# Kernel optimization log

Hardware: AMD Instinct MI355X
Metric: run time of the kernel (lower is better)

The kernel has to match this reference:

```python
import jax, jax.numpy as jnp
import numpy as np

B, N, EDGES = 16, 50000, 1600000
CLAMP_MIN, CLAMP_MAX = -10.0, 10.0
EPS = 1e-6


def setup_inputs() -> dict:
    key = jax.random.key(0)
    ks = jax.random.split(key, 8)
    return {
        "chem_influence": jax.random.normal(ks[0], (B, N), dtype=jnp.float32),
        "E": jax.random.normal(ks[1], (B, N), dtype=jnp.float32),
        "o_pre": jax.random.uniform(ks[2], (B, N), dtype=jnp.float32),
        "w": jax.random.normal(ks[3], (EDGES,), dtype=jnp.float32),
        "threshold": jax.random.uniform(ks[4], (N,), dtype=jnp.float32),
        "decay": jax.random.uniform(ks[5], (N,), dtype=jnp.float32),
        "src": jax.random.randint(ks[6], (EDGES,), 0, N, dtype=jnp.int32),
        "dst": jax.random.randint(ks[7], (EDGES,), 0, N, dtype=jnp.int32),
    }


def reference(chem_influence, E, o_pre, w, threshold, decay, src, dst):
    # Gap-junction currents: gather, sign-compare, weighted scatter-add.
    Oj = o_pre[:, src]                      # (B, EDGES) presynaptic outputs
    En = E[:, dst]                          # (B, EDGES) postsynaptic internal states
    sgn = jnp.where(Oj >= En, 1.0, -1.0)
    contrib = Oj * w * sgn                  # (B, EDGES)
    gj_sum = jnp.zeros_like(chem_influence).at[:, dst].add(contrib)  # (B, N)

    # Neuron dynamics (eqs 10, 11).
    S = jnp.clip(E + chem_influence + gj_sum, CLAMP_MIN, CLAMP_MAX)
    gt = S > threshold                      # broadcast (N,) over (B, N)
    mask = (~gt) & (jnp.abs(S - E) <= EPS)
    new_o = jax.nn.relu(S - threshold)
    new_e = jnp.where(gt, new_o, jnp.where(mask, E - decay, S))
    return (new_o, new_e)
```

## Files before the change

### kernel.cpp

```cpp
#include <hip/hip_runtime.h>

#define BATCH 16
#define NNODES 50000
#define NEDGES 1600000
#define BN (BATCH * NNODES)
#define CLAMP_LO -10.0f
#define CLAMP_HI 10.0f
#define EPS_V 1e-6f

#define BSZ 64
#define NBINS 782
#define CAPE 2816
#define RPT 11
#define NBLK_P 391
#define EPB 4096

__global__ __launch_bounds__(256) void prep_fused(
    const float* __restrict__ o_pre, const float* __restrict__ E,
    const int* __restrict__ src, const int* __restrict__ dst,
    const float* __restrict__ w,
    float* __restrict__ o_t, float* __restrict__ E_t,
    uint2* __restrict__ binned, int* __restrict__ gcur) {
    __shared__ int lh[NBINS];
    const int tid = threadIdx.x, bid = blockIdx.x;
    for (int i = tid; i < NBINS; i += 256) lh[i] = 0;

    const int4*   dst4 = (const int4*)dst;
    const int4*   src4 = (const int4*)src;
    const float4* w4   = (const float4*)w;
    const int e4base = bid * (EPB / 4);
    int4 d[4], s[4];
    float4 ww[4];
    bool val[4];
#pragma unroll
    for (int j = 0; j < 4; ++j) {
        int i4 = e4base + j * 256 + tid;
        val[j] = (i4 * 4 < NEDGES);
        if (val[j]) { d[j] = dst4[i4]; s[j] = src4[i4]; ww[j] = w4[i4]; }
    }

    if (tid < 128) {
        int t = bid * 128 + tid;
        if (t < NNODES) {
            float v[BATCH], u[BATCH];
#pragma unroll
            for (int b = 0; b < BATCH; ++b) {
                v[b] = o_pre[b * NNODES + t];
                u[b] = E[b * NNODES + t];
            }
            float4* op = (float4*)(o_t + (size_t)t * BATCH);
            float4* ep = (float4*)(E_t + (size_t)t * BATCH);
#pragma unroll
            for (int k = 0; k < 4; ++k) {
                op[k] = make_float4(v[4*k], v[4*k+1], v[4*k+2], v[4*k+3]);
                ep[k] = make_float4(u[4*k], u[4*k+1], u[4*k+2], u[4*k+3]);
            }
        }
    }
    __syncthreads();

#pragma unroll
    for (int j = 0; j < 4; ++j) {
        if (val[j]) {
            atomicAdd(&lh[d[j].x >> 6], 1);
            atomicAdd(&lh[d[j].y >> 6], 1);
            atomicAdd(&lh[d[j].z >> 6], 1);
            atomicAdd(&lh[d[j].w >> 6], 1);
        }
    }
    __syncthreads();

    for (int i = tid; i < NBINS; i += 256) {
        int c = lh[i];
        int base = c ? atomicAdd(&gcur[i], c) : 0;
        lh[i] = i * CAPE + base;
    }
    __syncthreads();

#pragma unroll
    for (int j = 0; j < 4; ++j) {
        if (val[j]) {
            int   dd[4] = {d[j].x, d[j].y, d[j].z, d[j].w};
            int   ss[4] = {s[j].x, s[j].y, s[j].z, s[j].w};
            float wv[4] = {ww[j].x, ww[j].y, ww[j].z, ww[j].w};
#pragma unroll
            for (int m = 0; m < 4; ++m) {
                int dn  = dd[m];
                int bin = dn >> 6;
                int pos = atomicAdd(&lh[bin], 1);
                if (pos < (bin + 1) * CAPE)
                    binned[pos] = make_uint2(
                        (unsigned)ss[m] | ((unsigned)(dn & 63) << 16),
                        __float_as_uint(wv[m]));
            }
        }
    }
}

__global__ __launch_bounds__(256, 4) void bin_gather6(
    const float* __restrict__ o_t, const float* __restrict__ E_t,
    const float* __restrict__ chem, const float* __restrict__ threshold,
    const float* __restrict__ decay, const int* __restrict__ gcur,
    const uint2* __restrict__ binned,
    float* __restrict__ out_o, float* __restrict__ out_e) {
    __shared__ int   cnt_l[BSZ];
    __shared__ int   offs[BSZ + 1];
    __shared__ uint2 eb[CAPE];
    const int k = blockIdx.x, tid = threadIdx.x;
    const int node0 = k * BSZ;
    const int nn = (NNODES - node0 < BSZ) ? (NNODES - node0) : BSZ;
    const int s0 = k * CAPE;
    int cnt = gcur[k];
    if (cnt > CAPE) cnt = CAPE;

    uint2 r[RPT];
    if (tid < BSZ) cnt_l[tid] = 0;
    __syncthreads();
#pragma unroll
    for (int j = 0; j < RPT; ++j) {
        int idx = tid + j * 256;
        if (idx < cnt) {
            uint2 p = binned[s0 + idx];
            r[j] = p;
            atomicAdd(&cnt_l[(p.x >> 16) & 63], 1);
        }
    }
    __syncthreads();

    if (tid < BSZ) {
        int c = cnt_l[tid];
        int v = c;
#pragma unroll
        for (int o = 1; o < BSZ; o <<= 1) {
            int u = __shfl_up(v, o);
            if (tid >= o) v += u;
        }
        offs[tid]  = v - c;
        cnt_l[tid] = v - c;
        if (tid == BSZ - 1) offs[BSZ] = cnt;
    }
    __syncthreads();

#pragma unroll
    for (int j = 0; j < RPT; ++j) {
        int idx = tid + j * 256;
        if (idx < cnt) {
            uint2 p = r[j];
            int pos = atomicAdd(&cnt_l[(p.x >> 16) & 63], 1);
            eb[pos] = p;
        }
    }
    __syncthreads();

    if (tid < nn * 4) {
        const int n  = tid >> 2;
        const int q  = (tid & 3) * 4;
        const int gn = node0 + n;
        const int e0 = offs[n], e1 = offs[n + 1];
        const float4 en = *(const float4*)(E_t + (size_t)gn * BATCH + q);
        const float th = threshold[gn];
        const float dc = decay[gn];
        float ch[4];
#pragma unroll
        for (int j = 0; j < 4; ++j) ch[j] = chem[(q + j) * NNODES + gn];

        float4 acc = make_float4(0.f, 0.f, 0.f, 0.f);
        int i = e0;
        for (; i + 2 <= e1; i += 2) {
            uint2 p0 = eb[i];
            uint2 p1 = eb[i + 1];
            float4 oj0 = *(const float4*)(o_t + (size_t)(p0.x & 0xFFFFu) * BATCH + q);
            float4 oj1 = *(const float4*)(o_t + (size_t)(p1.x & 0xFFFFu) * BATCH + q);
            float w0 = __uint_as_float(p0.y), nw0 = -w0;
            float w1 = __uint_as_float(p1.y), nw1 = -w1;
            acc.x = fmaf(oj0.x, (oj0.x >= en.x) ? w0 : nw0, acc.x);
            acc.y = fmaf(oj0.y, (oj0.y >= en.y) ? w0 : nw0, acc.y);
            acc.z = fmaf(oj0.z, (oj0.z >= en.z) ? w0 : nw0, acc.z);
            acc.w = fmaf(oj0.w, (oj0.w >= en.w) ? w0 : nw0, acc.w);
            acc.x = fmaf(oj1.x, (oj1.x >= en.x) ? w1 : nw1, acc.x);
            acc.y = fmaf(oj1.y, (oj1.y >= en.y) ? w1 : nw1, acc.y);
            acc.z = fmaf(oj1.z, (oj1.z >= en.z) ? w1 : nw1, acc.z);
            acc.w = fmaf(oj1.w, (oj1.w >= en.w) ? w1 : nw1, acc.w);
        }
        if (i < e1) {
            uint2 p0 = eb[i];
            float4 oj0 = *(const float4*)(o_t + (size_t)(p0.x & 0xFFFFu) * BATCH + q);
            float w0 = __uint_as_float(p0.y), nw0 = -w0;
            acc.x = fmaf(oj0.x, (oj0.x >= en.x) ? w0 : nw0, acc.x);
            acc.y = fmaf(oj0.y, (oj0.y >= en.y) ? w0 : nw0, acc.y);
            acc.z = fmaf(oj0.z, (oj0.z >= en.z) ? w0 : nw0, acc.z);
            acc.w = fmaf(oj0.w, (oj0.w >= en.w) ? w0 : nw0, acc.w);
        }

        float ev[4] = {en.x, en.y, en.z, en.w};
        float av[4] = {acc.x, acc.y, acc.z, acc.w};
#pragma unroll
        for (int j = 0; j < 4; ++j) {
            float e = ev[j];
            float S = e + ch[j] + av[j];
            S = fminf(fmaxf(S, CLAMP_LO), CLAMP_HI);
            float no = fmaxf(S - th, 0.0f);
            float ne;
            if (S > th) ne = no;
            else if (fabsf(S - e) <= EPS_V) ne = e - dc;
            else ne = S;
            out_o[(q + j) * NNODES + gn] = no;
            out_e[(q + j) * NNODES + gn] = ne;
        }
    }
}

__global__ void edge_scatter_dev(const float* __restrict__ o_pre, const float* __restrict__ E,
                                 const float* __restrict__ w, const int* __restrict__ src,
                                 const int* __restrict__ dst, float* __restrict__ gj) {
    int e = blockIdx.x * blockDim.x + threadIdx.x;
    if (e >= NEDGES) return;
    int s = src[e];
    int d = dst[e];
    float wv = w[e];
#pragma unroll
    for (int b = 0; b < BATCH; ++b) {
        float oj = o_pre[b * NNODES + s];
        float en = E[b * NNODES + d];
        atomicAdd(&gj[b * NNODES + d], (oj >= en) ? oj * wv : -oj * wv);
    }
}

__global__ void finalize_dev(const float* __restrict__ chem, const float* __restrict__ E,
                             const float* __restrict__ threshold, const float* __restrict__ decay,
                             float* __restrict__ out_o, float* __restrict__ out_e_gj) {
    int i = blockIdx.x * blockDim.x + threadIdx.x;
    if (i >= BN) return;
    int n = i % NNODES;
    float e = E[i];
    float S = e + chem[i] + out_e_gj[i];
    S = fminf(fmaxf(S, CLAMP_LO), CLAMP_HI);
    float th = threshold[n];
    float no = fmaxf(S - th, 0.0f);
    float ne;
    if (S > th) ne = no;
    else if (fabsf(S - e) <= EPS_V) ne = e - decay[n];
    else ne = S;
    out_o[i] = no;
    out_e_gj[i] = ne;
}

extern "C" void kernel_launch(void* const* d_in, const int* in_sizes, int n_in,
                              void* d_out, int out_size, void* d_ws, size_t ws_size,
                              hipStream_t stream) {
    const float* chem      = (const float*)d_in[0];
    const float* E         = (const float*)d_in[1];
    const float* o_pre     = (const float*)d_in[2];
    const float* w         = (const float*)d_in[3];
    const float* threshold = (const float*)d_in[4];
    const float* decay     = (const float*)d_in[5];
    const int*   src       = (const int*)d_in[6];
    const int*   dst       = (const int*)d_in[7];

    float* out_o = (float*)d_out;
    float* out_e = (float*)d_out + BN;

    const size_t OT_OFF  = 0;
    const size_t ET_OFF  = 3203072;
    const size_t BIN_OFF = 6406144;
    const size_t GC_OFF  = 24023040;
    const size_t need    = GC_OFF + (size_t)NBINS * sizeof(int);

    if (ws_size >= need) {
        char* ws = (char*)d_ws;
        float* o_t    = (float*)(ws + OT_OFF);
        float* E_t    = (float*)(ws + ET_OFF);
        uint2* binned = (uint2*)(ws + BIN_OFF);
        int*   gcur   = (int*)(ws + GC_OFF);

        hipMemsetAsync(gcur, 0, (size_t)NBINS * sizeof(int), stream);
        prep_fused<<<NBLK_P, 256, 0, stream>>>(o_pre, E, src, dst, w, o_t, E_t, binned, gcur);
        bin_gather6<<<NBINS, 256, 0, stream>>>(o_t, E_t, chem, threshold, decay,
                                               gcur, binned, out_o, out_e);
    } else {
        hipMemsetAsync(out_e, 0, (size_t)BN * sizeof(float), stream);
        edge_scatter_dev<<<(NEDGES + 255) / 256, 256, 0, stream>>>(o_pre, E, w, src, dst, out_e);
        finalize_dev<<<(BN + 255) / 256, 256, 0, stream>>>(chem, E, threshold, decay, out_o, out_e);
    }
}
```

Baseline: 125.3 us.

## Drop E transpose, read E directly in gather; halve edges per prep block

Removes the transposed copy of E from the prep kernel, so the gather kernel reads E from its original batch-major layout, the same way it already reads chem. The prep kernel now runs twice as many blocks with half the edges each, and all 256 threads take part in transposing o_pre, each writing a float4. The gather inner loop is unrolled by four edges to expose more independent loads. This saves one 3.2 MB write and its re-read, but the E reads in the gather become strided across batch rows, and the extra prep blocks mean more shared-histogram setup and more global bin atomics.

```diff
diff --git a/kernel.cpp b/kernel.cpp
--- a/kernel.cpp
+++ b/kernel.cpp
@@ -12,14 +12,14 @@
 #define NBINS 782
 #define CAPE 2816
 #define RPT 11
-#define NBLK_P 391
-#define EPB 4096
+#define NBLK_P 782
+#define EPB 2048
 
 __global__ __launch_bounds__(256) void prep_fused(
-    const float* __restrict__ o_pre, const float* __restrict__ E,
+    const float* __restrict__ o_pre,
     const int* __restrict__ src, const int* __restrict__ dst,
     const float* __restrict__ w,
-    float* __restrict__ o_t, float* __restrict__ E_t,
+    float* __restrict__ o_t,
     uint2* __restrict__ binned, int* __restrict__ gcur) {
     __shared__ int lh[NBINS];
     const int tid = threadIdx.x, bid = blockIdx.x;
@@ -29,38 +29,32 @@
     const int4*   src4 = (const int4*)src;
     const float4* w4   = (const float4*)w;
     const int e4base = bid * (EPB / 4);
-    int4 d[4], s[4];
-    float4 ww[4];
-    bool val[4];
-#pragma unroll
-    for (int j = 0; j < 4; ++j) {
+    int4 d[2], s[2];
+    float4 ww[2];
+    bool val[2];
+#pragma unroll
+    for (int j = 0; j < 2; ++j) {
         int i4 = e4base + j * 256 + tid;
-        val[j] = (i4 * 4 < NEDGES);
+        val[j] = (i4 < NEDGES / 4);
         if (val[j]) { d[j] = dst4[i4]; s[j] = src4[i4]; ww[j] = w4[i4]; }
     }
 
-    if (tid < 128) {
-        int t = bid * 128 + tid;
+    {
+        int t = bid * 64 + (tid >> 2);
+        int q = tid & 3;
         if (t < NNODES) {
-            float v[BATCH], u[BATCH];
-#pragma unroll
-            for (int b = 0; b < BATCH; ++b) {
-                v[b] = o_pre[b * NNODES + t];
-                u[b] = E[b * NNODES + t];
-            }
-            float4* op = (float4*)(o_t + (size_t)t * BATCH);
-            float4* ep = (float4*)(E_t + (size_t)t * BATCH);
-#pragma unroll
-            for (int k = 0; k < 4; ++k) {
-                op[k] = make_float4(v[4*k], v[4*k+1], v[4*k+2], v[4*k+3]);
-                ep[k] = make_float4(u[4*k], u[4*k+1], u[4*k+2], u[4*k+3]);
-            }
-        }
-    }
-    __syncthreads();
-
-#pragma unroll
-    for (int j = 0; j < 4; ++j) {
+            float v0 = o_pre[(q * 4 + 0) * NNODES + t];
+            float v1 = o_pre[(q * 4 + 1) * NNODES + t];
+            float v2 = o_pre[(q * 4 + 2) * NNODES + t];
+            float v3 = o_pre[(q * 4 + 3) * NNODES + t];
+            *(float4*)(o_t + (size_t)t * BATCH + q * 4) =
+                make_float4(v0, v1, v2, v3);
+        }
+    }
+    __syncthreads();
+
+#pragma unroll
+    for (int j = 0; j < 2; ++j) {
         if (val[j]) {
             atomicAdd(&lh[d[j].x >> 6], 1);
             atomicAdd(&lh[d[j].y >> 6], 1);
@@ -78,7 +72,7 @@
     __syncthreads();
 
 #pragma unroll
-    for (int j = 0; j < 4; ++j) {
+    for (int j = 0; j < 2; ++j) {
         if (val[j]) {
             int   dd[4] = {d[j].x, d[j].y, d[j].z, d[j].w};
             int   ss[4] = {s[j].x, s[j].y, s[j].z, s[j].w};
@@ -97,8 +91,8 @@
     }
 }
 
-__global__ __launch_bounds__(256, 4) void bin_gather6(
-    const float* __restrict__ o_t, const float* __restrict__ E_t,
+__global__ __launch_bounds__(256, 4) void bin_gather7(
+    const float* __restrict__ o_t, const float* __restrict__ E,
     const float* __restrict__ chem, const float* __restrict__ threshold,
     const float* __restrict__ decay, const int* __restrict__ gcur,
     const uint2* __restrict__ binned,
@@ -154,45 +148,42 @@
 
     if (tid < nn * 4) {
         const int n  = tid >> 2;
-        const int q  = (tid & 3) * 4;
+        const int q4 = (tid & 3) * 4;
         const int gn = node0 + n;
         const int e0 = offs[n], e1 = offs[n + 1];
-        const float4 en = *(const float4*)(E_t + (size_t)gn * BATCH + q);
+        float ev[4];
+#pragma unroll
+        for (int j = 0; j < 4; ++j) ev[j] = E[(q4 + j) * NNODES + gn];
         const float th = threshold[gn];
         const float dc = decay[gn];
         float ch[4];
 #pragma unroll
-        for (int j = 0; j < 4; ++j) ch[j] = chem[(q + j) * NNODES + gn];
+        for (int j = 0; j < 4; ++j) ch[j] = chem[(q4 + j) * NNODES + gn];
 
         float4 acc = make_float4(0.f, 0.f, 0.f, 0.f);
+#define ACC1(P)                                                                 \
+        {                                                                       \
+            float4 oj = *(const float4*)(o_t + (size_t)((P).x & 0xFFFFu) * BATCH + q4); \
+            float wv = __uint_as_float((P).y), nwv = -wv;                       \
+            acc.x = fmaf(oj.x, (oj.x >= ev[0]) ? wv : nwv, acc.x);              \
+            acc.y = fmaf(oj.y, (oj.y >= ev[1]) ? wv : nwv, acc.y);              \
+            acc.z = fmaf(oj.z, (oj.z >= ev[2]) ? wv : nwv, acc.z);              \
+            acc.w = fmaf(oj.w, (oj.w >= ev[3]) ? wv : nwv, acc.w);              \
+        }
         int i = e0;
-        for (; i + 2 <= e1; i += 2) {
+        for (; i + 4 <= e1; i += 4) {
             uint2 p0 = eb[i];
             uint2 p1 = eb[i + 1];
-            float4 oj0 = *(const float4*)(o_t + (size_t)(p0.x & 0xFFFFu) * BATCH + q);
-            float4 oj1 = *(const float4*)(o_t + (size_t)(p1.x & 0xFFFFu) * BATCH + q);
-            float w0 = __uint_as_float(p0.y), nw0 = -w0;
-            float w1 = __uint_as_float(p1.y), nw1 = -w1;
-            acc.x = fmaf(oj0.x, (oj0.x >= en.x) ? w0 : nw0, acc.x);
-            acc.y = fmaf(oj0.y, (oj0.y >= en.y) ? w0 : nw0, acc.y);
-            acc.z = fmaf(oj0.z, (oj0.z >= en.z) ? w0 : nw0, acc.z);
-            acc.w = fmaf(oj0.w, (oj0.w >= en.w) ? w0 : nw0, acc.w);
-            acc.x = fmaf(oj1.x, (oj1.x >= en.x) ? w1 : nw1, acc.x);
-            acc.y = fmaf(oj1.y, (oj1.y >= en.y) ? w1 : nw1, acc.y);
-            acc.z = fmaf(oj1.z, (oj1.z >= en.z) ? w1 : nw1, acc.z);
-            acc.w = fmaf(oj1.w, (oj1.w >= en.w) ? w1 : nw1, acc.w);
-        }
-        if (i < e1) {
+            uint2 p2 = eb[i + 2];
+            uint2 p3 = eb[i + 3];
+            ACC1(p0); ACC1(p1); ACC1(p2); ACC1(p3);
+        }
+        for (; i < e1; ++i) {
             uint2 p0 = eb[i];
-            float4 oj0 = *(const float4*)(o_t + (size_t)(p0.x & 0xFFFFu) * BATCH + q);
-            float w0 = __uint_as_float(p0.y), nw0 = -w0;
-            acc.x = fmaf(oj0.x, (oj0.x >= en.x) ? w0 : nw0, acc.x);
-            acc.y = fmaf(oj0.y, (oj0.y >= en.y) ? w0 : nw0, acc.y);
-            acc.z = fmaf(oj0.z, (oj0.z >= en.z) ? w0 : nw0, acc.z);
-            acc.w = fmaf(oj0.w, (oj0.w >= en.w) ? w0 : nw0, acc.w);
-        }
-
-        float ev[4] = {en.x, en.y, en.z, en.w};
+            ACC1(p0);
+        }
+#undef ACC1
+
         float av[4] = {acc.x, acc.y, acc.z, acc.w};
 #pragma unroll
         for (int j = 0; j < 4; ++j) {
@@ -204,8 +195,8 @@
             if (S > th) ne = no;
             else if (fabsf(S - e) <= EPS_V) ne = e - dc;
             else ne = S;
-            out_o[(q + j) * NNODES + gn] = no;
-            out_e[(q + j) * NNODES + gn] = ne;
+            out_o[(q4 + j) * NNODES + gn] = no;
+            out_e[(q4 + j) * NNODES + gn] = ne;
         }
     }
 }
@@ -261,21 +252,19 @@
     float* out_e = (float*)d_out + BN;
 
     const size_t OT_OFF  = 0;
-    const size_t ET_OFF  = 3203072;
-    const size_t BIN_OFF = 6406144;
-    const size_t GC_OFF  = 24023040;
+    const size_t BIN_OFF = 3203072;
+    const size_t GC_OFF  = 20819968;
     const size_t need    = GC_OFF + (size_t)NBINS * sizeof(int);
 
     if (ws_size >= need) {
         char* ws = (char*)d_ws;
         float* o_t    = (float*)(ws + OT_OFF);
-        float* E_t    = (float*)(ws + ET_OFF);
         uint2* binned = (uint2*)(ws + BIN_OFF);
         int*   gcur   = (int*)(ws + GC_OFF);
 
         hipMemsetAsync(gcur, 0, (size_t)NBINS * sizeof(int), stream);
-        prep_fused<<<NBLK_P, 256, 0, stream>>>(o_pre, E, src, dst, w, o_t, E_t, binned, gcur);
-        bin_gather6<<<NBINS, 256, 0, stream>>>(o_t, E_t, chem, threshold, decay,
+        prep_fused<<<NBLK_P, 256, 0, stream>>>(o_pre, src, dst, w, o_t, binned, gcur);
+        bin_gather7<<<NBINS, 256, 0, stream>>>(o_t, E, chem, threshold, decay,
                                                gcur, binned, out_o, out_e);
     } else {
         hipMemsetAsync(out_e, 0, (size_t)BN * sizeof(float), stream);
```

New measurement: 140.2 us. +11.9%, slower.
